# Performance work log

Hardware: AMD Instinct MI355X
Metric: run time of the kernel (lower is better)

The kernel has to match this reference:

```python
import jax, jax.numpy as jnp
import numpy as np

N_NODES = 100000
N_EDGES = 3200000
F_IN = 256
CUTOFF_DIST = 4.0
CUTOFF_ONSET = 3.8
D = 0.5 * (CUTOFF_DIST - CUTOFF_ONSET)  # 0.1
R = CUTOFF_DIST - D                      # 3.9


def setup_inputs() -> dict:
    key = jax.random.key(0)
    ks = jax.random.split(key, 8)
    node_features = jax.random.normal(ks[0], (N_NODES, F_IN), dtype=jnp.float32)
    bond_order = jax.random.uniform(ks[1], (N_EDGES,), dtype=jnp.float32)
    # scale to [0, 5) so the cutoff window [3.7, 4.1] is exercised
    bondlength = jax.random.uniform(ks[2], (N_EDGES,), dtype=jnp.float32) * 5.0
    src = jax.random.randint(ks[3], (N_EDGES,), 0, N_NODES, dtype=jnp.int64)
    dst = jax.random.randint(ks[4], (N_EDGES,), 0, N_NODES, dtype=jnp.int64)
    W_src = jax.random.normal(ks[5], (F_IN, 4), dtype=jnp.float32) * 0.05
    # bias init from the module: log([3264, 3.2394, 95.373, 1.3258])
    b_src = jnp.log(jnp.array([3264.0, 3.2394, 95.373, 1.3258], dtype=jnp.float32))
    W_dst = jax.random.normal(ks[6], (F_IN, 4), dtype=jnp.float32) * 0.05
    return {
        "node_features": node_features,
        "bond_order": bond_order,
        "bondlength": bondlength,
        "src": src,
        "dst": dst,
        "W_src": W_src,
        "b_src": b_src,
        "W_dst": W_dst,
    }


def _cutoff(r):
    c = jnp.where(r < R - D, 1.0, 0.5 - 0.5 * jnp.sin(jnp.pi * (r - R) / (2.0 * D)))
    return jnp.where(r > R + D, 0.0, c)


def reference(node_features, bond_order, bondlength, src, dst, W_src, b_src, W_dst):
    # per-node 4-vector projections
    e_src = node_features @ W_src + b_src          # [N, 4]
    e_dst = node_features @ W_dst                  # [N, 4]
    # gather to edges and combine (u_add_v), then exp
    params = jnp.exp(e_src[src] + e_dst[dst])      # [E, 4]
    f_repulse = params[:, 0] * jnp.exp(-params[:, 1] * bondlength)
    f_attract = params[:, 2] * jnp.exp(-params[:, 3] * bondlength)
    V_pair = _cutoff(bondlength) * (f_repulse - bond_order * f_attract)  # [E]
    # scatter-sum messages to destination nodes
    return jax.ops.segment_sum(V_pair, dst, num_segments=node_features.shape[0])
```

## Files before the change

kernel.cpp:

```cpp
#include <hip/hip_runtime.h>
#include <math.h>


#define F_IN 256
#define NB 49
#define BSH 11
#define BNODES 2048
#define SLOTS 16
#define NXCD 8
#define SC_T 512
#define SC_E 8
#define PBCAP 128
#define MAXK 16

typedef float fx4 __attribute__((ext_vector_type(4)));
typedef int ix4 __attribute__((ext_vector_type(4)));
typedef unsigned ux2 __attribute__((ext_vector_type(2)));
typedef unsigned ux4 __attribute__((ext_vector_type(4)));
typedef unsigned short usx4 __attribute__((ext_vector_type(4)));

__device__ __forceinline__ unsigned xcc_id() {
  unsigned x;
  asm("s_getreg_b32 %0, hwreg(HW_REG_XCC_ID)" : "=s"(x));
  return x & (NXCD - 1);
}

__device__ __forceinline__ unsigned short f2bf(float x) {
  const unsigned u = __float_as_uint(x);
  const unsigned r = u + 0x7fffu + ((u >> 16) & 1u);
  return (unsigned short)(r >> 16);
}
__device__ __forceinline__ float bf2f(unsigned short h) {
  return __uint_as_float((unsigned)h << 16);
}

__global__ __launch_bounds__(SC_T) void fused_kernel(
    const float* __restrict__ nf,
    const float* __restrict__ Wsrc,
    const float* __restrict__ bsrc,
    const float* __restrict__ Wdst,
    float* __restrict__ Psrc,
    float* __restrict__ Pdst,
    unsigned short* __restrict__ Pdst16,
    const float* __restrict__ bond_order,
    const float* __restrict__ bondlength,
    const int* __restrict__ src,
    const int* __restrict__ dst,
    ux2* __restrict__ region,
    unsigned* __restrict__ cntT,
    int n_nodes, int n_edges, int nsb, int npb) {
  __shared__ unsigned cnt[NB];
  __shared__ unsigned lofs[NB + 1];
  __shared__ ux2 stage[SC_T * SC_E];
  __shared__ unsigned char bkt8[SC_T * SC_E];

  const int bid = blockIdx.x;
  const int tid = threadIdx.x;
  const bool is_scatter = (nsb > 0) && (bid % 3 == 2);

  if (!is_scatter) {
    const int pidx = (nsb > 0) ? ((bid / 3) * 2 + (bid % 3)) : bid;
    if (pidx >= npb) return;
    const int gw = pidx * 8 + (tid >> 6);
    const int lane = tid & 63;
    const int node0 = gw * 8;
    if (node0 >= n_nodes) return;
    const int nm = min(8, n_nodes - node0);

    fx4 ws[4], wd[4];
#pragma unroll
    for (int t = 0; t < 4; ++t) {
      ws[t] = *reinterpret_cast<const fx4*>(Wsrc + (lane * 4 + t) * 4);
      wd[t] = *reinterpret_cast<const fx4*>(Wdst + (lane * 4 + t) * 4);
    }
    fx4 f[8];
#pragma unroll
    for (int m = 0; m < 8; ++m) {
      const int node = node0 + (m < nm ? m : 0);
      f[m] = *reinterpret_cast<const fx4*>(nf + (size_t)node * F_IN + lane * 4);
    }
    const int o = (lane & 1) * 4 + ((lane >> 1) & 1) * 2 + ((lane >> 2) & 1);
    const bool b1 = lane & 1, b2 = lane & 2, b4 = lane & 4;

#pragma unroll
    for (int m = 0; m < 8; ++m) {
      float a[8] = {0.f, 0.f, 0.f, 0.f, 0.f, 0.f, 0.f, 0.f};
#pragma unroll
      for (int t = 0; t < 4; ++t) {
        const float fv = f[m][t];
        a[0] += fv * ws[t].x; a[1] += fv * ws[t].y;
        a[2] += fv * ws[t].z; a[3] += fv * ws[t].w;
        a[4] += fv * wd[t].x; a[5] += fv * wd[t].y;
        a[6] += fv * wd[t].z; a[7] += fv * wd[t].w;
      }
      float s0 = b1 ? a[0] : a[4], s1 = b1 ? a[1] : a[5];
      float s2 = b1 ? a[2] : a[6], s3 = b1 ? a[3] : a[7];
      float r0 = __shfl_xor(s0, 1, 64), r1 = __shfl_xor(s1, 1, 64);
      float r2 = __shfl_xor(s2, 1, 64), r3 = __shfl_xor(s3, 1, 64);
      a[0] = (b1 ? a[4] : a[0]) + r0;
      a[1] = (b1 ? a[5] : a[1]) + r1;
      a[2] = (b1 ? a[6] : a[2]) + r2;
      a[3] = (b1 ? a[7] : a[3]) + r3;
      s0 = b2 ? a[0] : a[2]; s1 = b2 ? a[1] : a[3];
      r0 = __shfl_xor(s0, 2, 64); r1 = __shfl_xor(s1, 2, 64);
      a[0] = (b2 ? a[2] : a[0]) + r0;
      a[1] = (b2 ? a[3] : a[1]) + r1;
      s0 = b4 ? a[0] : a[1];
      r0 = __shfl_xor(s0, 4, 64);
      float v = (b4 ? a[1] : a[0]) + r0;
      v += __shfl_xor(v, 8, 64);
      v += __shfl_xor(v, 16, 64);
      v += __shfl_xor(v, 32, 64);

      if (m < nm && lane < 8) {
        const int node = node0 + m;
        if (o < 4) {
          Psrc[(size_t)node * 4 + o] = __expf(v + bsrc[o]);
        } else {
          const float e = __expf(v);
          if (Pdst16) Pdst16[(size_t)node * 4 + (o - 4)] = f2bf(e);
          else        Pdst[(size_t)node * 4 + (o - 4)] = e;
        }
      }
    }
    return;
  }

  const int sblk = bid / 3;
  if (tid < NB) cnt[tid] = 0;
  __syncthreads();

  const long long e0 = (long long)sblk * (SC_T * SC_E) + (long long)tid * SC_E;
  float rr[SC_E], bb[SC_E];
  int sc[SC_E], dl[SC_E], bk[SC_E];
  unsigned rk[SC_E];
  bool act[SC_E];

  if (e0 + SC_E <= n_edges) {
    const fx4 r0 = *reinterpret_cast<const fx4*>(bondlength + e0);
    const fx4 r1 = *reinterpret_cast<const fx4*>(bondlength + e0 + 4);
    const fx4 b0 = *reinterpret_cast<const fx4*>(bond_order + e0);
    const fx4 b1 = *reinterpret_cast<const fx4*>(bond_order + e0 + 4);
    const ix4 s0 = *reinterpret_cast<const ix4*>(src + e0);
    const ix4 s1 = *reinterpret_cast<const ix4*>(src + e0 + 4);
    const ix4 d0 = *reinterpret_cast<const ix4*>(dst + e0);
    const ix4 d1 = *reinterpret_cast<const ix4*>(dst + e0 + 4);
#pragma unroll
    for (int j = 0; j < 4; ++j) {
      rr[j] = r0[j]; rr[j + 4] = r1[j];
      bb[j] = b0[j]; bb[j + 4] = b1[j];
      sc[j] = s0[j]; sc[j + 4] = s1[j];
      const int d = d0[j], dh = d1[j];
      bk[j] = d >> BSH; dl[j] = d & (BNODES - 1);
      bk[j + 4] = dh >> BSH; dl[j + 4] = dh & (BNODES - 1);
    }
  } else {
#pragma unroll
    for (int j = 0; j < SC_E; ++j) {
      rr[j] = 1.0e9f; bb[j] = 0.f; sc[j] = 0; bk[j] = 0; dl[j] = 0;
    }
    for (int j = 0; j < SC_E; ++j) {
      const long long e = e0 + j;
      if (e < n_edges) {
        rr[j] = bondlength[e];
        bb[j] = bond_order[e];
        sc[j] = src[e];
        const int d = dst[e];
        bk[j] = d >> BSH; dl[j] = d & (BNODES - 1);
      }
    }
  }

#pragma unroll
  for (int j = 0; j < SC_E; ++j) {
    act[j] = rr[j] < 4.0f;
    if (act[j]) rk[j] = atomicAdd(&cnt[bk[j]], 1u);
  }
  __syncthreads();

  if (tid == 0) {
    unsigned run = 0;
#pragma unroll
    for (int b = 0; b < NB; ++b) { lofs[b] = run; run += cnt[b]; }
    lofs[NB] = run;
  }
  __syncthreads();

#pragma unroll
  for (int j = 0; j < SC_E; ++j) {
    if (!act[j]) continue;
    unsigned ru = (unsigned)(rr[j] * 16384.0f + 0.5f);
    ru = ru > 65535u ? 65535u : ru;
    unsigned bu = (unsigned)(bb[j] * 65535.0f + 0.5f);
    bu = bu > 65535u ? 65535u : bu;
    ux2 rec;
    rec.x = ((unsigned)sc[j] << BSH) | (unsigned)dl[j];
    rec.y = (ru << 16) | bu;
    const unsigned sidx = lofs[bk[j]] + rk[j];
    stage[sidx] = rec;
    bkt8[sidx] = (unsigned char)bk[j];
  }
  __syncthreads();

  const unsigned total = lofs[NB];
  for (unsigned i = tid; i < total; i += SC_T) {
    const int b = bkt8[i];
    const unsigned pos = i - lofs[b];
    if (pos < PBCAP)
      region[((size_t)b * nsb + sblk) * PBCAP + pos] = stage[i];
  }
  if (tid < NB) cntT[(size_t)tid * nsb + sblk] = cnt[tid];
}

__global__ __launch_bounds__(256) void accum_kernel(
    const ux2* __restrict__ region,
    const unsigned* __restrict__ cntT,
    const fx4* __restrict__ Psrc,
    const usx4* __restrict__ Pdst16,
    float* __restrict__ partial,
    int n_nodes, int nsb) {
  const int b = blockIdx.x / SLOTS;
  const int slot = blockIdx.x % SLOTS;
  __shared__ usx4 pdw16[BNODES];
  __shared__ float acc[BNODES];
  const int tid = threadIdx.x;
  const int wv = tid >> 6, lane = tid & 63;
  const int nbase = b << BSH;

  for (int j = tid; j < BNODES; j += 256) {
    const int n = nbase + j;
    pdw16[j] = (n < n_nodes) ? Pdst16[n] : usx4{0, 0, 0, 0};
    acc[j] = 0.f;
  }
  __syncthreads();

  const unsigned* cb = cntT + (size_t)b * nsb;
  const ux2* rb = region + (size_t)b * nsb * PBCAP;
  const int start = slot * 4 + wv;

  unsigned cs[MAXK];
#pragma unroll
  for (int k = 0; k < MAXK; ++k) {
    const int blk = start + 64 * k;
    cs[k] = (blk < nsb) ? cb[blk] : 0u;
  }

  const unsigned i0 = 2u * (unsigned)lane;
#pragma unroll
  for (int k = 0; k < MAXK; ++k) {
    const int blk = start + 64 * k;
    if (blk >= nsb) break;
    const unsigned c = min(cs[k], (unsigned)PBCAP);
    if (i0 >= c) continue;
    const ux4 rp =
        *reinterpret_cast<const ux4*>(rb + (size_t)blk * PBCAP + i0);
    const fx4 ps0 = Psrc[rp.x >> BSH];
    const bool h1 = (i0 + 1) < c;
    fx4 ps1;
    if (h1) ps1 = Psrc[rp.z >> BSH];

    {
      const int dl = rp.x & (BNODES - 1);
      const float r = (float)(rp.y >> 16) * (1.0f / 16384.0f);
      const float bo = (float)(rp.y & 0xffffu) * (1.0f / 65535.0f);
      const usx4 q = pdw16[dl];
      const float f_rep =
          (ps0.x * bf2f(q.x)) * __expf(-(ps0.y * bf2f(q.y)) * r);
      const float f_att =
          (ps0.z * bf2f(q.z)) * __expf(-(ps0.w * bf2f(q.w)) * r);
      float c1 = 1.0f;
      if (r > 3.8f) c1 = 0.5f - 0.5f * __sinf((float)M_PI * (r - 3.9f) * 5.0f);
      atomicAdd(&acc[dl], c1 * (f_rep - bo * f_att));
    }
    if (h1) {
      const int dl = rp.z & (BNODES - 1);
      const float r = (float)(rp.w >> 16) * (1.0f / 16384.0f);
      const float bo = (float)(rp.w & 0xffffu) * (1.0f / 65535.0f);
      const usx4 q = pdw16[dl];
      const float f_rep =
          (ps1.x * bf2f(q.x)) * __expf(-(ps1.y * bf2f(q.y)) * r);
      const float f_att =
          (ps1.z * bf2f(q.z)) * __expf(-(ps1.w * bf2f(q.w)) * r);
      float c1 = 1.0f;
      if (r > 3.8f) c1 = 0.5f - 0.5f * __sinf((float)M_PI * (r - 3.9f) * 5.0f);
      atomicAdd(&acc[dl], c1 * (f_rep - bo * f_att));
    }
  }
  __syncthreads();

  float* pout = partial + ((size_t)b * SLOTS + slot) * BNODES;
  for (int j = tid; j < BNODES; j += 256) pout[j] = acc[j];
}

__global__ __launch_bounds__(256) void reduce2_kernel(
    const float* __restrict__ partial, float* __restrict__ out, int n_nodes) {
  const int n = blockIdx.x * 256 + threadIdx.x;
  if (n >= n_nodes) return;
  const int b = n >> BSH;
  const int j = n & (BNODES - 1);
  const float* p = partial + (size_t)b * SLOTS * BNODES + j;
  float s = 0.f;
#pragma unroll
  for (int k = 0; k < SLOTS; ++k) s += p[(size_t)k * BNODES];
  out[n] = s;
}

__global__ __launch_bounds__(256) void edge_kernel_fb(
    const float* __restrict__ bond_order,
    const float* __restrict__ bondlength,
    const int* __restrict__ src,
    const int* __restrict__ dst,
    const fx4* __restrict__ Psrc,
    const fx4* __restrict__ Pdst,
    float* __restrict__ partial,
    int n_edges, int n_nodes) {
  float* myout = partial + (size_t)xcc_id() * n_nodes;
  const long long base = (long long)(blockIdx.x * blockDim.x + threadIdx.x) * 4;
  if (base >= n_edges) return;
  float rr[4], bb[4];
  int ss[4], dd[4];
  const int rem = (int)(((long long)n_edges - base) < 4 ? (n_edges - base) : 4);
  if (rem == 4) {
    const fx4 r4 = *reinterpret_cast<const fx4*>(bondlength + base);
    const fx4 b4 = *reinterpret_cast<const fx4*>(bond_order + base);
    const ix4 s4 = *reinterpret_cast<const ix4*>(src + base);
    const ix4 d4 = *reinterpret_cast<const ix4*>(dst + base);
#pragma unroll
    for (int j = 0; j < 4; ++j) {
      rr[j] = r4[j]; bb[j] = b4[j]; ss[j] = s4[j]; dd[j] = d4[j];
    }
  } else {
#pragma unroll
    for (int j = 0; j < 4; ++j) { rr[j] = 1e9f; bb[j] = 0.f; ss[j] = 0; dd[j] = 0; }
    for (int j = 0; j < rem; ++j) {
      rr[j] = bondlength[base + j]; bb[j] = bond_order[base + j];
      ss[j] = src[base + j]; dd[j] = dst[base + j];
    }
  }
#pragma unroll
  for (int j = 0; j < 4; ++j) {
    if (rr[j] >= 4.0f) continue;
    const fx4 es = Psrc[ss[j]];
    const fx4 ed = Pdst[dd[j]];
    const float r = rr[j];
    const float f_rep = (es.x * ed.x) * __expf(-(es.y * ed.y) * r);
    const float f_att = (es.z * ed.z) * __expf(-(es.w * ed.w) * r);
    float c = 1.0f;
    if (r > 3.8f) c = 0.5f - 0.5f * __sinf((float)M_PI * (r - 3.9f) * 5.0f);
    atomicAdd(&myout[dd[j]], c * (f_rep - bb[j] * f_att));
  }
}

__global__ __launch_bounds__(256) void reduce_fb_kernel(
    const float* __restrict__ partial, float* __restrict__ out, int n_nodes) {
  const int i = (blockIdx.x * blockDim.x + threadIdx.x) * 4;
  if (i >= n_nodes) return;
  if (i + 4 <= n_nodes) {
    fx4 s = *reinterpret_cast<const fx4*>(partial + i);
#pragma unroll
    for (int x = 1; x < NXCD; ++x)
      s += *reinterpret_cast<const fx4*>(partial + (size_t)x * n_nodes + i);
    *reinterpret_cast<fx4*>(out + i) = s;
  } else {
    for (int k = i; k < n_nodes; ++k) {
      float s = 0.f;
      for (int x = 0; x < NXCD; ++x) s += partial[(size_t)x * n_nodes + k];
      out[k] = s;
    }
  }
}

extern "C" void kernel_launch(void* const* d_in, const int* in_sizes, int n_in,
                              void* d_out, int out_size, void* d_ws,
                              size_t ws_size, hipStream_t stream) {
  const float* nf   = (const float*)d_in[0];
  const float* bo   = (const float*)d_in[1];
  const float* bl   = (const float*)d_in[2];
  const int*   src  = (const int*)d_in[3];
  const int*   dst  = (const int*)d_in[4];
  const float* Wsrc = (const float*)d_in[5];
  const float* bsrc = (const float*)d_in[6];
  const float* Wdst = (const float*)d_in[7];
  float* out = (float*)d_out;

  const int n_nodes = out_size;
  const int n_edges = in_sizes[1];

  const int nsb = (int)(((long long)n_edges + SC_T * SC_E - 1) / (SC_T * SC_E));
  const int npb = (n_nodes + 63) / 64;

  uint8_t* w = (uint8_t*)d_ws;
  const size_t pbytes = (size_t)n_nodes * 16;
  fx4* Psrc = (fx4*)w; w += pbytes;

  const size_t p16_b     = (((size_t)n_nodes * 8) + 255) & ~(size_t)255;
  const size_t region_b  = (size_t)NB * nsb * PBCAP * 8;
  const size_t cnt_b     = ((size_t)NB * nsb * 4 + 255) & ~(size_t)255;
  const size_t partial_b = (size_t)NB * SLOTS * BNODES * 4;
  const size_t need = pbytes + p16_b + region_b + cnt_b + partial_b + 256;
  const bool binned = (ws_size >= need) && (n_nodes <= NB * BNODES) &&
                      (n_nodes < (1 << 17)) && (nsb <= SLOTS * 4 * MAXK);

  if (binned) {
    unsigned short* Pdst16 = (unsigned short*)w; w += p16_b;
    ux2* region = (ux2*)w; w += region_b;
    unsigned* cntT = (unsigned*)w; w += cnt_b;
    float* partial = (float*)w;

    {
      const int half = (npb + 1) / 2;
      const int grid = 3 * (nsb > half ? nsb : half);
      fused_kernel<<<grid, SC_T, 0, stream>>>(
          nf, Wsrc, bsrc, Wdst, (float*)Psrc, nullptr, Pdst16,
          bo, bl, src, dst, region, cntT, n_nodes, n_edges, nsb, npb);
    }
    accum_kernel<<<NB * SLOTS, 256, 0, stream>>>(
        region, cntT, Psrc, (const usx4*)Pdst16, partial, n_nodes, nsb);
    reduce2_kernel<<<(n_nodes + 255) / 256, 256, 0, stream>>>(partial, out,
                                                              n_nodes);
  } else {
    fx4* Pdst = (fx4*)w; w += pbytes;
    float* partial = (float*)w;
    {
      fused_kernel<<<npb, SC_T, 0, stream>>>(
          nf, Wsrc, bsrc, Wdst, (float*)Psrc, (float*)Pdst, nullptr,
          bo, bl, src, dst, nullptr, nullptr, n_nodes, n_edges, 0, npb);
    }
    (void)hipMemsetAsync(partial, 0, (size_t)NXCD * n_nodes * sizeof(float),
                         stream);
    {
      const long long threads = ((long long)n_edges + 3) / 4;
      const int blocks = (int)((threads + 255) / 256);
      edge_kernel_fb<<<blocks, 256, 0, stream>>>(bo, bl, src, dst, Psrc, Pdst,
                                                 partial, n_edges, n_nodes);
    }
    reduce_fb_kernel<<<(n_nodes + 1023) / 1024, 256, 0, stream>>>(partial, out,
                                                                  n_nodes);
  }
}
```

Baseline: 67.41 us.

## Merge projection and scatter work into the same blocks instead of interleaved roles

Previously the fused kernel gave each block one role: two of every three blocks did node projection and the third did edge binning. Now every block first projects two 64-node groups (ppb=2) and then, if its index is below nsb, goes on to the scatter phase. This cuts the grid to a third and removes role dispatch by block index. In exchange, projection and scatter run one after the other inside a block rather than concurrently across blocks, and register pressure may rise from combining both paths. A guard is added so the binned path is only taken when the grid covers all projection groups.

After: 73.71 us. 1.09x slower.

```diff
diff --git a/kernel.cpp b/kernel.cpp
--- a/kernel.cpp
+++ b/kernel.cpp
@@ -48,7 +48,7 @@
     const int* __restrict__ dst,
     ux2* __restrict__ region,
     unsigned* __restrict__ cntT,
-    int n_nodes, int n_edges, int nsb, int npb) {
+    int n_nodes, int n_edges, int nsb, int npb, int ppb) {
   __shared__ unsigned cnt[NB];
   __shared__ unsigned lofs[NB + 1];
   __shared__ ux2 stage[SC_T * SC_E];
@@ -56,16 +56,13 @@
 
   const int bid = blockIdx.x;
   const int tid = threadIdx.x;
-  const bool is_scatter = (nsb > 0) && (bid % 3 == 2);
-
-  if (!is_scatter) {
-    const int pidx = (nsb > 0) ? ((bid / 3) * 2 + (bid % 3)) : bid;
-    if (pidx >= npb) return;
-    const int gw = pidx * 8 + (tid >> 6);
+  const bool do_scatter = (nsb > 0) && (bid < nsb);
+
+  if (do_scatter && tid < NB) cnt[tid] = 0;
+
+  {
     const int lane = tid & 63;
-    const int node0 = gw * 8;
-    if (node0 >= n_nodes) return;
-    const int nm = min(8, n_nodes - node0);
+    const int wv = tid >> 6;
 
     fx4 ws[4], wd[4];
 #pragma unroll
@@ -73,63 +70,72 @@
       ws[t] = *reinterpret_cast<const fx4*>(Wsrc + (lane * 4 + t) * 4);
       wd[t] = *reinterpret_cast<const fx4*>(Wdst + (lane * 4 + t) * 4);
     }
-    fx4 f[8];
-#pragma unroll
-    for (int m = 0; m < 8; ++m) {
-      const int node = node0 + (m < nm ? m : 0);
-      f[m] = *reinterpret_cast<const fx4*>(nf + (size_t)node * F_IN + lane * 4);
-    }
     const int o = (lane & 1) * 4 + ((lane >> 1) & 1) * 2 + ((lane >> 2) & 1);
     const bool b1 = lane & 1, b2 = lane & 2, b4 = lane & 4;
 
-#pragma unroll
-    for (int m = 0; m < 8; ++m) {
-      float a[8] = {0.f, 0.f, 0.f, 0.f, 0.f, 0.f, 0.f, 0.f};
-#pragma unroll
-      for (int t = 0; t < 4; ++t) {
-        const float fv = f[m][t];
-        a[0] += fv * ws[t].x; a[1] += fv * ws[t].y;
-        a[2] += fv * ws[t].z; a[3] += fv * ws[t].w;
-        a[4] += fv * wd[t].x; a[5] += fv * wd[t].y;
-        a[6] += fv * wd[t].z; a[7] += fv * wd[t].w;
+    for (int u = 0; u < ppb; ++u) {
+      const int pidx = bid * ppb + u;
+      if (pidx >= npb) break;
+      const int node0 = (pidx * 8 + wv) * 8;
+      if (node0 >= n_nodes) continue;
+      const int nm = min(8, n_nodes - node0);
+
+      fx4 f[8];
+#pragma unroll
+      for (int m = 0; m < 8; ++m) {
+        const int node = node0 + (m < nm ? m : 0);
+        f[m] =
+            *reinterpret_cast<const fx4*>(nf + (size_t)node * F_IN + lane * 4);
       }
-      float s0 = b1 ? a[0] : a[4], s1 = b1 ? a[1] : a[5];
-      float s2 = b1 ? a[2] : a[6], s3 = b1 ? a[3] : a[7];
-      float r0 = __shfl_xor(s0, 1, 64), r1 = __shfl_xor(s1, 1, 64);
-      float r2 = __shfl_xor(s2, 1, 64), r3 = __shfl_xor(s3, 1, 64);
-      a[0] = (b1 ? a[4] : a[0]) + r0;
-      a[1] = (b1 ? a[5] : a[1]) + r1;
-      a[2] = (b1 ? a[6] : a[2]) + r2;
-      a[3] = (b1 ? a[7] : a[3]) + r3;
-      s0 = b2 ? a[0] : a[2]; s1 = b2 ? a[1] : a[3];
-      r0 = __shfl_xor(s0, 2, 64); r1 = __shfl_xor(s1, 2, 64);
-      a[0] = (b2 ? a[2] : a[0]) + r0;
-      a[1] = (b2 ? a[3] : a[1]) + r1;
-      s0 = b4 ? a[0] : a[1];
-      r0 = __shfl_xor(s0, 4, 64);
-      float v = (b4 ? a[1] : a[0]) + r0;
-      v += __shfl_xor(v, 8, 64);
-      v += __shfl_xor(v, 16, 64);
-      v += __shfl_xor(v, 32, 64);
-
-      if (m < nm && lane < 8) {
-        const int node = node0 + m;
-        if (o < 4) {
-          Psrc[(size_t)node * 4 + o] = __expf(v + bsrc[o]);
-        } else {
-          const float e = __expf(v);
-          if (Pdst16) Pdst16[(size_t)node * 4 + (o - 4)] = f2bf(e);
-          else        Pdst[(size_t)node * 4 + (o - 4)] = e;
+
+#pragma unroll
+      for (int m = 0; m < 8; ++m) {
+        float a[8] = {0.f, 0.f, 0.f, 0.f, 0.f, 0.f, 0.f, 0.f};
+#pragma unroll
+        for (int t = 0; t < 4; ++t) {
+          const float fv = f[m][t];
+          a[0] += fv * ws[t].x; a[1] += fv * ws[t].y;
+          a[2] += fv * ws[t].z; a[3] += fv * ws[t].w;
+          a[4] += fv * wd[t].x; a[5] += fv * wd[t].y;
+          a[6] += fv * wd[t].z; a[7] += fv * wd[t].w;
+        }
+        float s0 = b1 ? a[0] : a[4], s1 = b1 ? a[1] : a[5];
+        float s2 = b1 ? a[2] : a[6], s3 = b1 ? a[3] : a[7];
+        float r0 = __shfl_xor(s0, 1, 64), r1 = __shfl_xor(s1, 1, 64);
+        float r2 = __shfl_xor(s2, 1, 64), r3 = __shfl_xor(s3, 1, 64);
+        a[0] = (b1 ? a[4] : a[0]) + r0;
+        a[1] = (b1 ? a[5] : a[1]) + r1;
+        a[2] = (b1 ? a[6] : a[2]) + r2;
+        a[3] = (b1 ? a[7] : a[3]) + r3;
+        s0 = b2 ? a[0] : a[2]; s1 = b2 ? a[1] : a[3];
+        r0 = __shfl_xor(s0, 2, 64); r1 = __shfl_xor(s1, 2, 64);
+        a[0] = (b2 ? a[2] : a[0]) + r0;
+        a[1] = (b2 ? a[3] : a[1]) + r1;
+        s0 = b4 ? a[0] : a[1];
+        r0 = __shfl_xor(s0, 4, 64);
+        float v = (b4 ? a[1] : a[0]) + r0;
+        v += __shfl_xor(v, 8, 64);
+        v += __shfl_xor(v, 16, 64);
+        v += __shfl_xor(v, 32, 64);
+
+        if (m < nm && lane < 8) {
+          const int node = node0 + m;
+          if (o < 4) {
+            Psrc[(size_t)node * 4 + o] = __expf(v + bsrc[o]);
+          } else {
+            const float e = __expf(v);
+            if (Pdst16) Pdst16[(size_t)node * 4 + (o - 4)] = f2bf(e);
+            else        Pdst[(size_t)node * 4 + (o - 4)] = e;
+          }
         }
       }
     }
-    return;
-  }
-
-  const int sblk = bid / 3;
-  if (tid < NB) cnt[tid] = 0;
-  __syncthreads();
-
+  }
+
+  if (!do_scatter) return;
+  __syncthreads();
+
+  const int sblk = bid;
   const long long e0 = (long long)sblk * (SC_T * SC_E) + (long long)tid * SC_E;
   float rr[SC_E], bb[SC_E];
   int sc[SC_E], dl[SC_E], bk[SC_E];
@@ -399,7 +405,8 @@
   const size_t partial_b = (size_t)NB * SLOTS * BNODES * 4;
   const size_t need = pbytes + p16_b + region_b + cnt_b + partial_b + 256;
   const bool binned = (ws_size >= need) && (n_nodes <= NB * BNODES) &&
-                      (n_nodes < (1 << 17)) && (nsb <= SLOTS * 4 * MAXK);
+                      (n_nodes < (1 << 17)) && (nsb <= SLOTS * 4 * MAXK) &&
+                      (nsb * 2 + 2 > npb);
 
   if (binned) {
     unsigned short* Pdst16 = (unsigned short*)w; w += p16_b;
@@ -408,11 +415,10 @@
     float* partial = (float*)w;
 
     {
-      const int half = (npb + 1) / 2;
-      const int grid = 3 * (nsb > half ? nsb : half);
+      const int grid = (nsb > (npb + 1) / 2) ? nsb : (npb + 1) / 2;
       fused_kernel<<<grid, SC_T, 0, stream>>>(
           nf, Wsrc, bsrc, Wdst, (float*)Psrc, nullptr, Pdst16,
-          bo, bl, src, dst, region, cntT, n_nodes, n_edges, nsb, npb);
+          bo, bl, src, dst, region, cntT, n_nodes, n_edges, nsb, npb, 2);
     }
     accum_kernel<<<NB * SLOTS, 256, 0, stream>>>(
         region, cntT, Psrc, (const usx4*)Pdst16, partial, n_nodes, nsb);
@@ -424,7 +430,7 @@
     {
       fused_kernel<<<npb, SC_T, 0, stream>>>(
           nf, Wsrc, bsrc, Wdst, (float*)Psrc, (float*)Pdst, nullptr,
-          bo, bl, src, dst, nullptr, nullptr, n_nodes, n_edges, 0, npb);
+          bo, bl, src, dst, nullptr, nullptr, n_nodes, n_edges, 0, npb, 1);
     }
     (void)hipMemsetAsync(partial, 0, (size_t)NXCD * n_nodes * sizeof(float),
                          stream);
```
